# Optimization experiments

Measured on AMD Instinct MI355X. Metric: run time of the kernel, lower is better.

Reference implementation:

```python
import jax, jax.numpy as jnp
import numpy as np
import math

EMB_DIM = 2048
N_HEAD = 16
HEAD_DIM = EMB_DIM // N_HEAD
BATCH = 4
SEQ = 2048
ROPE_BASE = 10000.0


def apply_rope(x):
    # x: [B, S, H, D]; torchtune-style interleaved rotary embedding
    B, S, H, D = x.shape
    inv_freq = 1.0 / (ROPE_BASE ** (jnp.arange(0, D, 2, dtype=jnp.float32) / D))  # [D/2]
    angles = jnp.arange(S, dtype=jnp.float32)[:, None] * inv_freq[None, :]        # [S, D/2]
    cos = jnp.cos(angles)[None, :, None, :]  # [1,S,1,D/2]
    sin = jnp.sin(angles)[None, :, None, :]
    x1 = x[..., 0::2]
    x2 = x[..., 1::2]
    r1 = x1 * cos - x2 * sin
    r2 = x2 * cos + x1 * sin
    return jnp.stack([r1, r2], axis=-1).reshape(B, S, H, D)


def setup_inputs() -> dict:
    key = jax.random.key(0)
    ks = jax.random.split(key, 5)
    scale = 1.0 / math.sqrt(EMB_DIM)
    return {
        "x": jax.random.normal(ks[0], (BATCH, SEQ, EMB_DIM), dtype=jnp.float32),
        "Wq": jax.random.normal(ks[1], (EMB_DIM, EMB_DIM), dtype=jnp.float32) * scale,
        "Wk": jax.random.normal(ks[2], (EMB_DIM, EMB_DIM), dtype=jnp.float32) * scale,
        "Wv": jax.random.normal(ks[3], (EMB_DIM, EMB_DIM), dtype=jnp.float32) * scale,
        "Wo": jax.random.normal(ks[4], (EMB_DIM, EMB_DIM), dtype=jnp.float32) * scale,
    }


def reference(x, Wq, Wk, Wv, Wo) -> jnp.ndarray:
    B, S, _ = x.shape
    # nn.Linear(weight W) computes x @ W.T
    xq = (x @ Wq.T).reshape(B, S, N_HEAD, HEAD_DIM)
    xk = (x @ Wk.T).reshape(B, S, N_HEAD, HEAD_DIM)
    xv = (x @ Wv.T).reshape(B, S, N_HEAD, HEAD_DIM)
    xq = apply_rope(xq)
    xk = apply_rope(xk)
    # [B,H,S,D]
    q = xq.transpose(0, 2, 1, 3)
    k = xk.transpose(0, 2, 1, 3)
    v = xv.transpose(0, 2, 1, 3)
    scores = jnp.einsum("bhqd,bhkd->bhqk", q, k) / math.sqrt(HEAD_DIM)
    causal = jnp.tril(jnp.ones((S, S), dtype=bool))
    scores = jnp.where(causal[None, None], scores, -jnp.inf)
    attn = jax.nn.softmax(scores.astype(jnp.float32), axis=-1).astype(q.dtype)
    ctx = jnp.einsum("bhqk,bhkd->bhqd", attn, v)
    ctx = ctx.transpose(0, 2, 1, 3).reshape(B, S, EMB_DIM)
    return ctx @ Wo.T
```

## Files before the change

kernel.cpp:

```cpp
#include <hip/hip_runtime.h>
#include <hip/hip_fp16.h>

#define EMB 2048
#define NH 16
#define HD 128
#define BATCH 4
#define SEQ 2048
#define MROWS (BATCH * SEQ)

typedef __attribute__((ext_vector_type(8))) _Float16 f16x8;
typedef __attribute__((ext_vector_type(4))) float f32x4;

typedef __attribute__((address_space(3))) unsigned int lds_u32_t;
typedef const __attribute__((address_space(1))) unsigned int glb_u32_t;

__device__ __forceinline__ void async_copy16(void* lds, const void* g) {
    __builtin_amdgcn_global_load_lds((glb_u32_t*)g, (lds_u32_t*)lds, 16, 0, 0);
}

__global__ void cvt_f32_f16(const float* __restrict__ in, __half* __restrict__ out, int n4) {
    int i = blockIdx.x * 256 + threadIdx.x;
    if (i < n4) {
        float4 v = ((const float4*)in)[i];
        __half2 a, b;
        a.x = __float2half(v.x); a.y = __float2half(v.y);
        b.x = __float2half(v.z); b.y = __float2half(v.w);
        ((__half2*)out)[2 * i]     = a;
        ((__half2*)out)[2 * i + 1] = b;
    }
}

__device__ __forceinline__ void gemm_mainloop(const __half* __restrict__ A,
                                              const __half* __restrict__ B,
                                              int m0, int n0,
                                              short* sA, short* sB,
                                              f32x4 acc[4][4]) {
    const int tid  = threadIdx.x;
    const int wave = tid >> 6;
    const int lane = tid & 63;
    const int wr = wave >> 1, wc = wave & 1;
    const int frow = lane & 15;
    const int fk   = (lane >> 4) * 8;
    const int r0 = tid >> 2;
    const int cb = (tid & 3) * 16;
    const char* gA = (const char*)A;
    const char* gB = (const char*)B;
    char* lA = (char*)sA;
    char* lB = (char*)sB;
    const int off0 = wave * 1024;
    const int off1 = 4096 + wave * 1024;

    for (int kt = 0; kt < EMB; kt += 32) {
        size_t kb = (size_t)kt * 2;
        async_copy16(lA + off0, gA + ((size_t)(m0 + r0) * EMB) * 2 + kb + cb);
        async_copy16(lA + off1, gA + ((size_t)(m0 + 64 + r0) * EMB) * 2 + kb + cb);
        async_copy16(lB + off0, gB + ((size_t)(n0 + r0) * EMB) * 2 + kb + cb);
        async_copy16(lB + off1, gB + ((size_t)(n0 + 64 + r0) * EMB) * 2 + kb + cb);
        __syncthreads();

        f16x8 af[4], bf[4];
#pragma unroll
        for (int i = 0; i < 4; i++)
            af[i] = *(const f16x8*)&sA[(wr * 64 + i * 16 + frow) * 32 + fk];
#pragma unroll
        for (int i = 0; i < 4; i++)
            bf[i] = *(const f16x8*)&sB[(wc * 64 + i * 16 + frow) * 32 + fk];
#pragma unroll
        for (int mi = 0; mi < 4; mi++)
#pragma unroll
            for (int ni = 0; ni < 4; ni++)
                acc[mi][ni] = __builtin_amdgcn_mfma_f32_16x16x32_f16(af[mi], bf[ni], acc[mi][ni], 0, 0, 0);
        __syncthreads();
    }
}

__global__ __launch_bounds__(256) void gemm_qkv(const __half* __restrict__ X,
                                                const __half* __restrict__ Wq,
                                                const __half* __restrict__ Wk,
                                                const __half* __restrict__ Wv,
                                                __half* __restrict__ Q,
                                                __half* __restrict__ K,
                                                __half* __restrict__ V) {
    __shared__ short sA[128 * 32];
    __shared__ short sB[128 * 32];
    const int mblk = blockIdx.x;
    const int nb   = blockIdx.y;
    const int wsel = nb >> 4;
    const int nloc = (nb & 15) * 128;
    const __half* W = (wsel == 0) ? Wq : ((wsel == 1) ? Wk : Wv);

    f32x4 z = {0.f, 0.f, 0.f, 0.f};
    f32x4 acc[4][4];
#pragma unroll
    for (int i = 0; i < 4; i++)
#pragma unroll
        for (int j = 0; j < 4; j++) acc[i][j] = z;

    gemm_mainloop(X, W, mblk * 128, nloc, sA, sB, acc);

    const int lane = threadIdx.x & 63;
    const int wave = threadIdx.x >> 6;
    const int wr = wave >> 1, wc = wave & 1;
    const int q4 = lane >> 4;
    __half* Obuf = (wsel == 0) ? Q : ((wsel == 1) ? K : V);
    const bool rope = (wsel < 2);

#pragma unroll
    for (int ni = 0; ni < 4; ni++) {
        int n = nloc + wc * 64 + ni * 16 + (lane & 15);
        int h = n >> 7, d = n & 127;
        float invf = rope ? __expf(-((float)(d & ~1)) * (9.210340371976184f / 128.0f)) : 0.f;
#pragma unroll
        for (int mi = 0; mi < 4; mi++) {
#pragma unroll
            for (int r = 0; r < 4; r++) {
                int m = mblk * 128 + wr * 64 + mi * 16 + q4 * 4 + r;
                int b = m >> 11, s = m & 2047;
                float v = acc[mi][ni][r];
                float res;
                if (rope) {
                    float p = __shfl_xor(v, 1);
                    float ang = (float)s * invf;
                    float sn, cs;
                    __sincosf(ang, &sn, &cs);
                    if ((lane & 1) == 0) res = v * cs - p * sn;
                    else                 res = v * cs + p * sn;
                } else {
                    res = v;
                }
                float pr = __shfl_xor(res, 1);
                if ((lane & 1) == 0) {
                    __half2 hv;
                    hv.x = __float2half(res);
                    hv.y = __float2half(pr);
                    size_t off = ((size_t)(b * NH + h) * SEQ + s) * HD + d;
                    *(__half2*)(Obuf + off) = hv;
                }
            }
        }
    }
}

__global__ __launch_bounds__(256) void transpose_v(const __half* __restrict__ V,
                                                   __half* __restrict__ Vt) {
    __shared__ short t[64 * 65];
    const int st = blockIdx.x & 31;
    const int dt = (blockIdx.x >> 5) & 1;
    const int bh = blockIdx.y;
    const int tid = threadIdx.x;
    const __half* Vh = V + (size_t)bh * SEQ * HD;
    __half* Vo = Vt + (size_t)bh * SEQ * HD;
#pragma unroll
    for (int k = 0; k < 2; k++) {
        int id = k * 256 + tid;
        int r = id >> 3, c8 = id & 7;
        f16x8 v = *(const f16x8*)(Vh + (size_t)(st * 64 + r) * HD + dt * 64 + c8 * 8);
#pragma unroll
        for (int e = 0; e < 8; e++) t[r * 65 + c8 * 8 + e] = ((short*)&v)[e];
    }
    __syncthreads();
#pragma unroll
    for (int k = 0; k < 2; k++) {
        int id = k * 256 + tid;
        int dr = id >> 3, sc8 = id & 7;
        f16x8 v;
#pragma unroll
        for (int e = 0; e < 8; e++) ((short*)&v)[e] = t[(sc8 * 8 + e) * 65 + dr];
        *(f16x8*)(Vo + (size_t)(dt * 64 + dr) * SEQ + st * 64 + sc8 * 8) = v;
    }
}

__global__ __launch_bounds__(256, 3) void attn_kernel(const __half* __restrict__ Q,
                                                      const __half* __restrict__ K,
                                                      const __half* __restrict__ Vt,
                                                      __half* __restrict__ CTX) {
    __shared__ short sK[64 * 128];
    __shared__ short sV[128 * 64];
    __shared__ short sP[4][16 * 64];
    const int disp  = blockIdx.y * 16 + blockIdx.x;
    const int wid   = (disp & 7) * 128 + (disp >> 3);
    const int pairx = wid & 15;
    const int bh    = wid >> 4;
    const int b = bh >> 4, h = bh & 15;
    const int tid = threadIdx.x;
    const int wave = tid >> 6, lane = tid & 63;
    const int fr = lane & 15, q4 = lane >> 4;
    const size_t headoff = (size_t)bh * SEQ * HD;
    const __half* Qh = Q + headoff;
    const __half* Kh = K + headoff;
    const __half* Vth = Vt + headoff;
    short* sPw = &sP[wave][0];

    f32x4 z = {0.f, 0.f, 0.f, 0.f};

#pragma unroll 1
    for (int pass = 0; pass < 2; pass++) {
        const int qt = pass ? pairx : (31 - pairx);
        const int nk = qt + 1;

        f16x8 qf[4];
#pragma unroll
        for (int ds = 0; ds < 4; ds++) {
            qf[ds] = *(const f16x8*)(Qh + (size_t)(qt * 64 + wave * 16 + fr) * HD + ds * 32 + q4 * 8);
            qf[ds] = qf[ds] * (_Float16)0.08838834764831845f;
        }

        f32x4 accO[8];
#pragma unroll
        for (int i = 0; i < 8; i++) accO[i] = z;
        float mrow[4], lrow[4];
#pragma unroll
        for (int r = 0; r < 4; r++) { mrow[r] = -INFINITY; lrow[r] = 0.f; }

        f16x8 kpre[4], vpre[4];
#pragma unroll
        for (int j = 0; j < 4; j++) {
            int id = j * 256 + tid;
            int row = id >> 4, c = id & 15;
            kpre[j] = *(const f16x8*)(Kh + (size_t)row * HD + c * 8);
        }
#pragma unroll
        for (int j = 0; j < 4; j++) {
            int id = j * 256 + tid;
            int d = id >> 3, c = id & 7;
            vpre[j] = *(const f16x8*)(Vth + (size_t)d * SEQ + c * 8);
        }

        for (int kt = 0; kt < nk; kt++) {
            __syncthreads();
#pragma unroll
            for (int j = 0; j < 4; j++) {
                int id = j * 256 + tid;
                int row = id >> 4, c = id & 15;
                *(f16x8*)&sK[row * 128 + ((c ^ (row & 15)) * 8)] = kpre[j];
            }
#pragma unroll
            for (int j = 0; j < 4; j++) {
                int id = j * 256 + tid;
                int d = id >> 3, c = id & 7;
                *(f16x8*)&sV[d * 64 + ((c ^ (d & 7)) * 8)] = vpre[j];
            }
            __syncthreads();

            if (kt + 1 < nk) {
                int kbase = (kt + 1) * 64;
#pragma unroll
                for (int j = 0; j < 4; j++) {
                    int id = j * 256 + tid;
                    int row = id >> 4, c = id & 15;
                    kpre[j] = *(const f16x8*)(Kh + (size_t)(kbase + row) * HD + c * 8);
                }
#pragma unroll
                for (int j = 0; j < 4; j++) {
                    int id = j * 256 + tid;
                    int d = id >> 3, c = id & 7;
                    vpre[j] = *(const f16x8*)(Vth + (size_t)d * SEQ + kbase + c * 8);
                }
            }

            f32x4 accS[4];
#pragma unroll
            for (int i = 0; i < 4; i++) accS[i] = z;
            __builtin_amdgcn_s_setprio(1);
#pragma unroll
            for (int ds = 0; ds < 4; ds++) {
                f16x8 kf[4];
#pragma unroll
                for (int ni = 0; ni < 4; ni++)
                    kf[ni] = *(const f16x8*)&sK[(ni * 16 + fr) * 128 + (((ds * 4 + q4) ^ fr) * 8)];
#pragma unroll
                for (int ni = 0; ni < 4; ni++)
                    accS[ni] = __builtin_amdgcn_mfma_f32_16x16x32_f16(qf[ds], kf[ni], accS[ni], 0, 0, 0);
            }
            __builtin_amdgcn_s_setprio(0);

            if (kt == qt) {
#pragma unroll
                for (int ni = 0; ni < 4; ni++) {
                    int kcol = ni * 16 + fr;
#pragma unroll
                    for (int r = 0; r < 4; r++) {
                        int qrow = wave * 16 + q4 * 4 + r;
                        if (kcol > qrow) accS[ni][r] = -INFINITY;
                    }
                }
            }

#pragma unroll
            for (int r = 0; r < 4; r++) {
                float mold = mrow[r];
                float mx = mold;
#pragma unroll
                for (int ni = 0; ni < 4; ni++) mx = fmaxf(mx, accS[ni][r]);
#pragma unroll
                for (int off = 1; off < 16; off <<= 1)
                    mx = fmaxf(mx, __shfl_xor(mx, off));
                float alpha = __expf(mold - mx);
                mrow[r] = mx;
                float rs = 0.f;
#pragma unroll
                for (int ni = 0; ni < 4; ni++) {
                    float p = __expf(accS[ni][r] - mx);
                    rs += p;
                    accS[ni][r] = p;
                }
#pragma unroll
                for (int off = 1; off < 16; off <<= 1)
                    rs += __shfl_xor(rs, off);
                lrow[r] = lrow[r] * alpha + rs;
#pragma unroll
                for (int di = 0; di < 8; di++)
                    accO[di][r] *= alpha;
            }

#pragma unroll
            for (int ni = 0; ni < 4; ni++)
#pragma unroll
                for (int r = 0; r < 4; r++) {
                    float p = accS[ni][r];
                    float pp = __shfl_xor(p, 1);
                    if ((lane & 1) == 0) {
                        int row = q4 * 4 + r;
                        int col = ni * 16 + fr;
                        int xc = (col >> 3) ^ (row & 7);
                        __half2 h2;
                        h2.x = __float2half(p);
                        h2.y = __float2half(pp);
                        *(__half2*)&sPw[row * 64 + xc * 8 + (col & 7)] = h2;
                    }
                }

            __builtin_amdgcn_s_setprio(1);
#pragma unroll
            for (int ns = 0; ns < 2; ns++) {
                f16x8 pf = *(const f16x8*)&sPw[fr * 64 + (((ns * 4 + q4) ^ (fr & 7)) * 8)];
#pragma unroll
                for (int di = 0; di < 8; di++) {
                    f16x8 vf = *(const f16x8*)&sV[(di * 16 + fr) * 64 + (((ns * 4 + q4) ^ (fr & 7)) * 8)];
                    accO[di] = __builtin_amdgcn_mfma_f32_16x16x32_f16(pf, vf, accO[di], 0, 0, 0);
                }
            }
            __builtin_amdgcn_s_setprio(0);
        }

        float linv[4];
#pragma unroll
        for (int r = 0; r < 4; r++) linv[r] = 1.f / lrow[r];

#pragma unroll
        for (int di = 0; di < 8; di++)
#pragma unroll
            for (int r = 0; r < 4; r++) {
                float o = accO[di][r] * linv[r];
                float po = __shfl_xor(o, 1);
                if ((lane & 1) == 0) {
                    int srow = qt * 64 + wave * 16 + q4 * 4 + r;
                    int d = di * 16 + fr;
                    size_t off = ((size_t)(b * SEQ + srow)) * EMB + h * HD + d;
                    __half2 h2;
                    h2.x = __float2half(o);
                    h2.y = __float2half(po);
                    *(__half2*)&CTX[off] = h2;
                }
            }
    }
}

__global__ __launch_bounds__(256) void gemm_out(const __half* __restrict__ CTX,
                                                const __half* __restrict__ Wo,
                                                float* __restrict__ out) {
    __shared__ short sA[128 * 32];
    __shared__ short sB[128 * 32];
    f32x4 z = {0.f, 0.f, 0.f, 0.f};
    f32x4 acc[4][4];
#pragma unroll
    for (int i = 0; i < 4; i++)
#pragma unroll
        for (int j = 0; j < 4; j++) acc[i][j] = z;

    gemm_mainloop(CTX, Wo, blockIdx.x * 128, blockIdx.y * 128, sA, sB, acc);

    const int lane = threadIdx.x & 63;
    const int wave = threadIdx.x >> 6;
    const int wr = wave >> 1, wc = wave & 1;
    const int q4 = lane >> 4;
#pragma unroll
    for (int mi = 0; mi < 4; mi++)
#pragma unroll
        for (int ni = 0; ni < 4; ni++)
#pragma unroll
            for (int r = 0; r < 4; r++) {
                int m = blockIdx.x * 128 + wr * 64 + mi * 16 + q4 * 4 + r;
                int n = blockIdx.y * 128 + wc * 64 + ni * 16 + (lane & 15);
                out[(size_t)m * EMB + n] = acc[mi][ni][r];
            }
}

extern "C" void kernel_launch(void* const* d_in, const int* in_sizes, int n_in,
                              void* d_out, int out_size, void* d_ws, size_t ws_size,
                              hipStream_t stream) {
    const float* x  = (const float*)d_in[0];
    const float* Wq = (const float*)d_in[1];
    const float* Wk = (const float*)d_in[2];
    const float* Wv = (const float*)d_in[3];
    const float* Wo = (const float*)d_in[4];
    float* out = (float*)d_out;

    char* ws = (char*)d_ws;
    size_t off = 0;
    const size_t QKV_ELEMS = (size_t)MROWS * EMB;
    __half* Xh  = (__half*)(ws + off); off += QKV_ELEMS * 2;
    __half* Wqh = (__half*)(ws + off); off += (size_t)EMB * EMB * 2;
    __half* Wkh = (__half*)(ws + off); off += (size_t)EMB * EMB * 2;
    __half* Wvh = (__half*)(ws + off); off += (size_t)EMB * EMB * 2;
    __half* Woh = (__half*)(ws + off); off += (size_t)EMB * EMB * 2;
    __half* Qb  = (__half*)(ws + off); off += QKV_ELEMS * 2;
    __half* Kb  = (__half*)(ws + off); off += QKV_ELEMS * 2;
    __half* Vb  = (__half*)(ws + off); off += QKV_ELEMS * 2;
    __half* Vtb = (__half*)(ws + off); off += QKV_ELEMS * 2;
    __half* Cb  = Xh;

    cvt_f32_f16<<<16384, 256, 0, stream>>>(x,  Xh,  4194304);
    cvt_f32_f16<<<4096,  256, 0, stream>>>(Wq, Wqh, 1048576);
    cvt_f32_f16<<<4096,  256, 0, stream>>>(Wk, Wkh, 1048576);
    cvt_f32_f16<<<4096,  256, 0, stream>>>(Wv, Wvh, 1048576);
    cvt_f32_f16<<<4096,  256, 0, stream>>>(Wo, Woh, 1048576);

    gemm_qkv<<<dim3(64, 48), 256, 0, stream>>>(Xh, Wqh, Wkh, Wvh, Qb, Kb, Vb);
    transpose_v<<<dim3(64, 64), 256, 0, stream>>>(Vb, Vtb);
    attn_kernel<<<dim3(16, 64), 256, 0, stream>>>(Qb, Kb, Vtb, Cb);
    gemm_out<<<dim3(64, 16), 256, 0, stream>>>(Cb, Woh, out);
}
```

Measured before the change: 857.1 us.

## Triple-buffer GEMM mainloop, swizzle LDS, fuse V transpose and conversion launches

The shared GEMM mainloop now uses a three-stage LDS ring. Async global-to-LDS copies are issued two tiles ahead and waited on with explicit vmcnt counts and a single barrier per tile. An XOR swizzle on the 16-byte column slots is meant to reduce LDS bank conflicts. The QKV GEMM writes V directly in transposed layout, which removes the separate transpose kernel and one intermediate buffer, and the five conversion launches are merged into one. The extra LDS per block may lower occupancy, and the transposed V stores are narrow 8-byte writes strided by SEQ.

```diff
diff --git a/kernel.cpp b/kernel.cpp
--- a/kernel.cpp
+++ b/kernel.cpp
@@ -9,6 +9,7 @@
 #define MROWS (BATCH * SEQ)
 
 typedef __attribute__((ext_vector_type(8))) _Float16 f16x8;
+typedef __attribute__((ext_vector_type(4))) _Float16 f16x4;
 typedef __attribute__((ext_vector_type(4))) float f32x4;
 
 typedef __attribute__((address_space(3))) unsigned int lds_u32_t;
@@ -18,16 +19,31 @@
     __builtin_amdgcn_global_load_lds((glb_u32_t*)g, (lds_u32_t*)lds, 16, 0, 0);
 }
 
-__global__ void cvt_f32_f16(const float* __restrict__ in, __half* __restrict__ out, int n4) {
-    int i = blockIdx.x * 256 + threadIdx.x;
-    if (i < n4) {
-        float4 v = ((const float4*)in)[i];
-        __half2 a, b;
-        a.x = __float2half(v.x); a.y = __float2half(v.y);
-        b.x = __float2half(v.z); b.y = __float2half(v.w);
-        ((__half2*)out)[2 * i]     = a;
-        ((__half2*)out)[2 * i + 1] = b;
+__global__ void cvt_all(const float* __restrict__ x,  const float* __restrict__ wq,
+                        const float* __restrict__ wk, const float* __restrict__ wv,
+                        const float* __restrict__ wo,
+                        __half* __restrict__ xh,  __half* __restrict__ wqh,
+                        __half* __restrict__ wkh, __half* __restrict__ wvh,
+                        __half* __restrict__ woh) {
+    int bid = blockIdx.x;
+    const float* s;
+    __half* d;
+    int idx;
+    if (bid < 16384) {
+        s = x; d = xh; idx = bid * 256 + threadIdx.x;
+    } else {
+        int b2 = bid - 16384;
+        int w = b2 >> 12;
+        s = (w == 0) ? wq : (w == 1) ? wk : (w == 2) ? wv : wo;
+        d = (w == 0) ? wqh : (w == 1) ? wkh : (w == 2) ? wvh : woh;
+        idx = (b2 & 4095) * 256 + threadIdx.x;
     }
+    float4 v = ((const float4*)s)[idx];
+    __half2 a, b;
+    a.x = __float2half(v.x); a.y = __float2half(v.y);
+    b.x = __float2half(v.z); b.y = __float2half(v.w);
+    ((__half2*)d)[2 * idx]     = a;
+    ((__half2*)d)[2 * idx + 1] = b;
 }
 
 __device__ __forceinline__ void gemm_mainloop(const __half* __restrict__ A,
@@ -40,38 +56,59 @@
     const int lane = tid & 63;
     const int wr = wave >> 1, wc = wave & 1;
     const int frow = lane & 15;
-    const int fk   = (lane >> 4) * 8;
-    const int r0 = tid >> 2;
-    const int cb = (tid & 3) * 16;
-    const char* gA = (const char*)A;
-    const char* gB = (const char*)B;
+    const int q4   = lane >> 4;
+    const int r0   = tid >> 2;
+    const int csw  = ((tid & 3) ^ (r0 & 3)) * 16;
+    const char* gA = (const char*)A + (size_t)(m0 + r0) * (EMB * 2) + csw;
+    const char* gB = (const char*)B + (size_t)(n0 + r0) * (EMB * 2) + csw;
+    const size_t rstep = (size_t)64 * EMB * 2;
     char* lA = (char*)sA;
     char* lB = (char*)sB;
-    const int off0 = wave * 1024;
-    const int off1 = 4096 + wave * 1024;
-
-    for (int kt = 0; kt < EMB; kt += 32) {
-        size_t kb = (size_t)kt * 2;
-        async_copy16(lA + off0, gA + ((size_t)(m0 + r0) * EMB) * 2 + kb + cb);
-        async_copy16(lA + off1, gA + ((size_t)(m0 + 64 + r0) * EMB) * 2 + kb + cb);
-        async_copy16(lB + off0, gB + ((size_t)(n0 + r0) * EMB) * 2 + kb + cb);
-        async_copy16(lB + off1, gB + ((size_t)(n0 + 64 + r0) * EMB) * 2 + kb + cb);
-        __syncthreads();
-
+    const int ldst = tid * 16;
+
+#define STAGE_TILE(t, b) do {                                          \
+        size_t ko = (size_t)(t) * 64;                                  \
+        async_copy16(lA + (b) * 8192 + ldst,        gA + ko);          \
+        async_copy16(lA + (b) * 8192 + 4096 + ldst, gA + rstep + ko);  \
+        async_copy16(lB + (b) * 8192 + ldst,        gB + ko);          \
+        async_copy16(lB + (b) * 8192 + 4096 + ldst, gB + rstep + ko);  \
+    } while (0)
+
+    const int nt = EMB / 32;
+    STAGE_TILE(0, 0);
+    STAGE_TILE(1, 1);
+
+    int cb = 0;
+    for (int t = 0; t < nt; ++t) {
+        if (t < nt - 1) asm volatile("s_waitcnt vmcnt(4)" ::: "memory");
+        else            asm volatile("s_waitcnt vmcnt(0)" ::: "memory");
+        asm volatile("" ::: "memory");
+        __builtin_amdgcn_s_barrier();
+        asm volatile("" ::: "memory");
+
+        const short* bufA = sA + cb * 4096;
+        const short* bufB = sB + cb * 4096;
         f16x8 af[4], bf[4];
+        const int slot = (q4 ^ (frow & 3)) * 8;
 #pragma unroll
         for (int i = 0; i < 4; i++)
-            af[i] = *(const f16x8*)&sA[(wr * 64 + i * 16 + frow) * 32 + fk];
+            af[i] = *(const f16x8*)&bufA[(wr * 64 + i * 16 + frow) * 32 + slot];
 #pragma unroll
         for (int i = 0; i < 4; i++)
-            bf[i] = *(const f16x8*)&sB[(wc * 64 + i * 16 + frow) * 32 + fk];
+            bf[i] = *(const f16x8*)&bufB[(wc * 64 + i * 16 + frow) * 32 + slot];
 #pragma unroll
         for (int mi = 0; mi < 4; mi++)
 #pragma unroll
             for (int ni = 0; ni < 4; ni++)
                 acc[mi][ni] = __builtin_amdgcn_mfma_f32_16x16x32_f16(af[mi], bf[ni], acc[mi][ni], 0, 0, 0);
-        __syncthreads();
+
+        if (t + 2 < nt) {
+            int sb = cb + 2; if (sb >= 3) sb -= 3;
+            STAGE_TILE(t + 2, sb);
+        }
+        cb = (cb == 2) ? 0 : cb + 1;
     }
+#undef STAGE_TILE
 }
 
 __global__ __launch_bounds__(256) void gemm_qkv(const __half* __restrict__ X,
@@ -80,9 +117,9 @@
                                                 const __half* __restrict__ Wv,
                                                 __half* __restrict__ Q,
                                                 __half* __restrict__ K,
-                                                __half* __restrict__ V) {
-    __shared__ short sA[128 * 32];
-    __shared__ short sB[128 * 32];
+                                                __half* __restrict__ Vt) {
+    __shared__ short sA[3 * 128 * 32];
+    __shared__ short sB[3 * 128 * 32];
     const int mblk = blockIdx.x;
     const int nb   = blockIdx.y;
     const int wsel = nb >> 4;
@@ -102,14 +139,31 @@
     const int wave = threadIdx.x >> 6;
     const int wr = wave >> 1, wc = wave & 1;
     const int q4 = lane >> 4;
-    __half* Obuf = (wsel == 0) ? Q : ((wsel == 1) ? K : V);
-    const bool rope = (wsel < 2);
-
+
+    if (wsel == 2) {
+#pragma unroll
+        for (int ni = 0; ni < 4; ni++) {
+            int n = nloc + wc * 64 + ni * 16 + (lane & 15);
+            int h = n >> 7, d = n & 127;
+#pragma unroll
+            for (int mi = 0; mi < 4; mi++) {
+                int m = mblk * 128 + wr * 64 + mi * 16 + q4 * 4;
+                int b = m >> 11, s = m & 2047;
+                f16x4 hv;
+#pragma unroll
+                for (int r = 0; r < 4; r++) hv[r] = (_Float16)acc[mi][ni][r];
+                *(f16x4*)(Vt + ((size_t)(b * NH + h) * HD + d) * SEQ + s) = hv;
+            }
+        }
+        return;
+    }
+
+    __half* Obuf = (wsel == 0) ? Q : K;
 #pragma unroll
     for (int ni = 0; ni < 4; ni++) {
         int n = nloc + wc * 64 + ni * 16 + (lane & 15);
         int h = n >> 7, d = n & 127;
-        float invf = rope ? __expf(-((float)(d & ~1)) * (9.210340371976184f / 128.0f)) : 0.f;
+        float invf = __expf(-((float)(d & ~1)) * (9.210340371976184f / 128.0f));
 #pragma unroll
         for (int mi = 0; mi < 4; mi++) {
 #pragma unroll
@@ -117,17 +171,13 @@
                 int m = mblk * 128 + wr * 64 + mi * 16 + q4 * 4 + r;
                 int b = m >> 11, s = m & 2047;
                 float v = acc[mi][ni][r];
+                float p = __shfl_xor(v, 1);
+                float ang = (float)s * invf;
+                float sn, cs;
+                __sincosf(ang, &sn, &cs);
                 float res;
-                if (rope) {
-                    float p = __shfl_xor(v, 1);
-                    float ang = (float)s * invf;
-                    float sn, cs;
-                    __sincosf(ang, &sn, &cs);
-                    if ((lane & 1) == 0) res = v * cs - p * sn;
-                    else                 res = v * cs + p * sn;
-                } else {
-                    res = v;
-                }
+                if ((lane & 1) == 0) res = v * cs - p * sn;
+                else                 res = v * cs + p * sn;
                 float pr = __shfl_xor(res, 1);
                 if ((lane & 1) == 0) {
                     __half2 hv;
@@ -138,35 +188,6 @@
                 }
             }
         }
-    }
-}
-
-__global__ __launch_bounds__(256) void transpose_v(const __half* __restrict__ V,
-                                                   __half* __restrict__ Vt) {
-    __shared__ short t[64 * 65];
-    const int st = blockIdx.x & 31;
-    const int dt = (blockIdx.x >> 5) & 1;
-    const int bh = blockIdx.y;
-    const int tid = threadIdx.x;
-    const __half* Vh = V + (size_t)bh * SEQ * HD;
-    __half* Vo = Vt + (size_t)bh * SEQ * HD;
-#pragma unroll
-    for (int k = 0; k < 2; k++) {
-        int id = k * 256 + tid;
-        int r = id >> 3, c8 = id & 7;
-        f16x8 v = *(const f16x8*)(Vh + (size_t)(st * 64 + r) * HD + dt * 64 + c8 * 8);
-#pragma unroll
-        for (int e = 0; e < 8; e++) t[r * 65 + c8 * 8 + e] = ((short*)&v)[e];
-    }
-    __syncthreads();
-#pragma unroll
-    for (int k = 0; k < 2; k++) {
-        int id = k * 256 + tid;
-        int dr = id >> 3, sc8 = id & 7;
-        f16x8 v;
-#pragma unroll
-        for (int e = 0; e < 8; e++) ((short*)&v)[e] = t[(sc8 * 8 + e) * 65 + dr];
-        *(f16x8*)(Vo + (size_t)(dt * 64 + dr) * SEQ + st * 64 + sc8 * 8) = v;
     }
 }
 
@@ -369,8 +390,8 @@
 __global__ __launch_bounds__(256) void gemm_out(const __half* __restrict__ CTX,
                                                 const __half* __restrict__ Wo,
                                                 float* __restrict__ out) {
-    __shared__ short sA[128 * 32];
-    __shared__ short sB[128 * 32];
+    __shared__ short sA[3 * 128 * 32];
+    __shared__ short sB[3 * 128 * 32];
     f32x4 z = {0.f, 0.f, 0.f, 0.f};
     f32x4 acc[4][4];
 #pragma unroll
@@ -416,18 +437,12 @@
     __half* Woh = (__half*)(ws + off); off += (size_t)EMB * EMB * 2;
     __half* Qb  = (__half*)(ws + off); off += QKV_ELEMS * 2;
     __half* Kb  = (__half*)(ws + off); off += QKV_ELEMS * 2;
-    __half* Vb  = (__half*)(ws + off); off += QKV_ELEMS * 2;
     __half* Vtb = (__half*)(ws + off); off += QKV_ELEMS * 2;
     __half* Cb  = Xh;
 
-    cvt_f32_f16<<<16384, 256, 0, stream>>>(x,  Xh,  4194304);
-    cvt_f32_f16<<<4096,  256, 0, stream>>>(Wq, Wqh, 1048576);
-    cvt_f32_f16<<<4096,  256, 0, stream>>>(Wk, Wkh, 1048576);
-    cvt_f32_f16<<<4096,  256, 0, stream>>>(Wv, Wvh, 1048576);
-    cvt_f32_f16<<<4096,  256, 0, stream>>>(Wo, Woh, 1048576);
-
-    gemm_qkv<<<dim3(64, 48), 256, 0, stream>>>(Xh, Wqh, Wkh, Wvh, Qb, Kb, Vb);
-    transpose_v<<<dim3(64, 64), 256, 0, stream>>>(Vb, Vtb);
+    cvt_all<<<32768, 256, 0, stream>>>(x, Wq, Wk, Wv, Wo, Xh, Wqh, Wkh, Wvh, Woh);
+
+    gemm_qkv<<<dim3(64, 48), 256, 0, stream>>>(Xh, Wqh, Wkh, Wvh, Qb, Kb, Vtb);
     attn_kernel<<<dim3(16, 64), 256, 0, stream>>>(Qb, Kb, Vtb, Cb);
     gemm_out<<<dim3(64, 16), 256, 0, stream>>>(Cb, Woh, out);
 }
```

Result: faster. 777.1 us (-9.3%).
